# Kernel tuning notes

Hardware: AMD Instinct MI355X
Metric: run time of the kernel (lower is better)

## Reference

```python
import jax, jax.numpy as jnp
import numpy as np

LN_EPS = 1e-5


def _pos_embed_2d(w, h, c, dtype=jnp.float32):
    # matches build_2d_sincos_position_embedding: meshgrid indexing='xy' -> (h, w) grids
    grid_w = jnp.arange(w, dtype=jnp.float32)
    grid_h = jnp.arange(h, dtype=jnp.float32)
    gw, gh = jnp.meshgrid(grid_w, grid_h, indexing='xy')  # each (h, w)
    pos_dim = c // 4
    omega = 1.0 / (10000.0 ** (jnp.arange(pos_dim, dtype=jnp.float32) / pos_dim))
    out_w = gw.reshape(-1, 1) * omega[None]  # (h*w, pos_dim)
    out_h = gh.reshape(-1, 1) * omega[None]
    pe = jnp.concatenate([jnp.sin(out_w), jnp.cos(out_w), jnp.sin(out_h), jnp.cos(out_h)], axis=1)
    return pe.astype(dtype)  # (h*w, c)


def setup_inputs() -> dict:
    key = jax.random.key(0)
    k1, k2 = jax.random.split(key)
    N, C, H, W = 16, 256, 40, 40
    x = jax.random.normal(k1, (N, C, H, W), dtype=jnp.float32)
    ln_w = jnp.ones((C,), dtype=jnp.float32)
    ln_b = jnp.zeros((C,), dtype=jnp.float32)
    qkv_w = jax.random.normal(k2, (3 * C, C), dtype=jnp.float32) * 0.02  # 1x1 conv weight
    qkv_b = jnp.zeros((3 * C,), dtype=jnp.float32)
    gamma = jnp.ones((1,), dtype=jnp.float32)
    return {"x": x, "ln_w": ln_w, "ln_b": ln_b, "qkv_w": qkv_w, "qkv_b": qkv_b, "gamma": gamma}


def reference(x, ln_w, ln_b, qkv_w, qkv_b, gamma):
    N, C, H, W = x.shape
    scale = C ** (-0.5)
    identity = x

    # LayerNorm over channels (computed in NHWC like the torch permute dance)
    xh = jnp.transpose(x, (0, 2, 3, 1))  # (N, H, W, C)
    mu = jnp.mean(xh, axis=-1, keepdims=True)
    var = jnp.mean(jnp.square(xh - mu), axis=-1, keepdims=True)
    xn = (xh - mu) * jax.lax.rsqrt(var + LN_EPS) * ln_w + ln_b

    # 1x1 conv == per-pixel linear
    qkv = jnp.einsum('nhwc,oc->nhwo', xn, qkv_w) + qkv_b  # (N, H, W, 3C)
    qkv = qkv.reshape(N, H * W, 3 * C)
    q, k, v = jnp.split(qkv, 3, axis=-1)  # each (N, HW, C)

    pe = _pos_embed_2d(W, H, C, x.dtype)  # (HW, C)
    q = q + pe
    k = k + pe

    attn = jax.nn.softmax(jnp.einsum('nqc,nkc->nqk', q, k) * scale, axis=-1)
    out = jnp.einsum('nqk,nkc->nqc', attn, v)  # (N, HW, C)
    out = jnp.transpose(out, (0, 2, 1)).reshape(N, C, H, W)
    return identity + gamma[0] * out
```

## Files before the change

### kernel.cpp

```cpp
#include <hip/hip_runtime.h>
#include <hip/hip_bf16.h>

typedef float f32x4 __attribute__((ext_vector_type(4)));
typedef float f32x16 __attribute__((ext_vector_type(16)));
typedef __bf16 v8bf __attribute__((ext_vector_type(8)));
typedef unsigned short ushortx4 __attribute__((ext_vector_type(4)));
typedef unsigned short ushortx8 __attribute__((ext_vector_type(8)));
typedef unsigned int uint4v __attribute__((ext_vector_type(4)));

#define NIMG 16
#define CCH  256
#define HWP  1600
#define APIT 264

__device__ __forceinline__ unsigned short f2bf(float f) {
  unsigned int u = __builtin_bit_cast(unsigned int, f);
  u = (u + 0x7FFFu + ((u >> 16) & 1u)) >> 16;
  return (unsigned short)u;
}

__device__ __forceinline__ f32x4 mfma16(v8bf a, v8bf b, f32x4 c) {
  return __builtin_amdgcn_mfma_f32_16x16x32_bf16(a, b, c, 0, 0, 0);
}

__device__ __forceinline__ unsigned cvtpk(float a, float b) {
  unsigned r;
  asm("v_cvt_pk_bf16_f32 %0, %1, %2" : "=v"(r) : "v"(a), "v"(b));
  return r;
}
#define PSWAP(a, b) asm("v_permlane32_swap_b32 %0, %1" : "+v"(a), "+v"(b))

__global__ void prep_kernel(const float* __restrict__ qkv_w,
                            float* __restrict__ pe,
                            unsigned short* __restrict__ w_frag) {
  int tid = blockIdx.x * blockDim.x + threadIdx.x;
  int nthr = gridDim.x * blockDim.x;
  for (int i = tid; i < 768 * 256; i += nthr) {
    int o = i >> 8, c = i & 255;
    int tile = o >> 4, lr = o & 15;
    int ks = c >> 5, lg = (c >> 3) & 3, e = c & 7;
    w_frag[(((size_t)tile * 8 + ks) * 64 + lg * 16 + lr) * 8 + e] = f2bf(qkv_w[i]);
  }
  const float c1 = 9.210340371976184f / 64.f;
  for (int i = tid; i < HWP * 256; i += nthr) {
    int p = i >> 8, c = i & 255;
    int j = p % 40, ii = p / 40;
    int tt = c & 63;
    float omega = expf(-(float)tt * c1);
    float coord = (c < 128) ? (float)j : (float)ii;
    float a = coord * omega;
    pe[i] = ((c & 64) == 0) ? sinf(a) : cosf(a);
  }
}

__global__ __launch_bounds__(512, 4) void ln_qkv_kernel(
    const float* __restrict__ x, const float* __restrict__ ln_w, const float* __restrict__ ln_b,
    const unsigned short* __restrict__ w_frag, const float* __restrict__ qkv_b,
    const float* __restrict__ pe,
    unsigned short* __restrict__ q_arr, unsigned short* __restrict__ k_arr,
    unsigned short* __restrict__ v_arr) {
  __shared__ unsigned short buf[64][APIT];
  __shared__ float red_s[8][64], red_q[8][64];
  __shared__ float mu_s[64], rs_s[64];

  int t = threadIdx.x;
  int n = blockIdx.x / 25, pt = blockIdx.x % 25;
  int pix0 = pt * 64;
  int p = t & 63, g = t >> 6;
  const float* xb = x + (size_t)n * CCH * HWP + pix0;

  {
    float sum = 0.f, sq = 0.f;
#pragma unroll
    for (int i = 0; i < 32; ++i) {
      float v = xb[(size_t)(g * 32 + i) * HWP + p];
      sum += v; sq += v * v;
    }
    red_s[g][p] = sum; red_q[g][p] = sq;
  }
  __syncthreads();
  if (t < 64) {
    float s = 0.f, q2 = 0.f;
#pragma unroll
    for (int gg = 0; gg < 8; ++gg) { s += red_s[gg][t]; q2 += red_q[gg][t]; }
    float mu = s * (1.f / 256.f);
    float var = q2 * (1.f / 256.f) - mu * mu;
    mu_s[t] = mu;
    rs_s[t] = rsqrtf(var + 1e-5f);
  }
  __syncthreads();
  {
    float mu = mu_s[p], rs = rs_s[p];
#pragma unroll
    for (int i4 = 0; i4 < 8; ++i4) {
      int c0 = g * 32 + i4 * 4;
      f32x4 lw = *(const f32x4*)&ln_w[c0];
      f32x4 lb = *(const f32x4*)&ln_b[c0];
      ushortx4 pk;
#pragma unroll
      for (int r = 0; r < 4; ++r) {
        float v = xb[(size_t)(c0 + r) * HWP + p];
        pk[r] = f2bf((v - mu) * rs * lw[r] + lb[r]);
      }
      *(ushortx4*)&buf[p][c0] = pk;
    }
  }
  __syncthreads();

  int w = t >> 6, l = t & 63, lr = l & 15, lg = l >> 4;
  f32x4 acc[6][4];
#pragma unroll
  for (int nf = 0; nf < 6; ++nf)
#pragma unroll
    for (int mi = 0; mi < 4; ++mi) acc[nf][mi] = (f32x4){0.f, 0.f, 0.f, 0.f};

#pragma unroll
  for (int ks = 0; ks < 8; ++ks) {
    v8bf bF[4];
#pragma unroll
    for (int mi = 0; mi < 4; ++mi)
      bF[mi] = *(const v8bf*)&buf[mi * 16 + lr][ks * 32 + lg * 8];
#pragma unroll
    for (int nf = 0; nf < 6; ++nf) {
      int tile = w + nf * 8;
      v8bf wf = *(const v8bf*)&w_frag[(((size_t)tile * 8 + ks) * 64 + l) * 8];
#pragma unroll
      for (int mi = 0; mi < 4; ++mi) acc[nf][mi] = mfma16(wf, bF[mi], acc[nf][mi]);
    }
  }

  int lgh = lg >> 1, lgl = lg & 1;
#pragma unroll
  for (int nf = 0; nf < 2; ++nf) {
    int tile = w + nf * 8;
    f32x4 bi = *(const f32x4*)&qkv_b[tile * 16 + lg * 4];
#pragma unroll
    for (int mi = 0; mi < 4; ++mi) {
      int pix = pix0 + mi * 16 + lr;
      f32x4 pev = *(const f32x4*)&pe[(size_t)pix * 256 + tile * 16 + lg * 4];
      f32x4 vv = (acc[nf][mi] + bi + pev) * 0.0625f;
      ushortx4 pk = {f2bf(vv[0]), f2bf(vv[1]), f2bf(vv[2]), f2bf(vv[3])};
      int qt = pix >> 5, l31 = pix & 31;
      size_t ad = ((((size_t)n * 50 + qt) * 16 + tile) * 2 + lgh) * 256 + l31 * 8 + lgl * 4;
      *(ushortx4*)&q_arr[ad] = pk;
    }
  }
#pragma unroll
  for (int nf = 2; nf < 4; ++nf) {
    int tile = w + nf * 8;
    int dt = tile - 16;
    f32x4 bi = *(const f32x4*)&qkv_b[tile * 16 + lg * 4];
#pragma unroll
    for (int mi = 0; mi < 4; ++mi) {
      int pix = pix0 + mi * 16 + lr;
      f32x4 pev = *(const f32x4*)&pe[(size_t)pix * 256 + dt * 16 + lg * 4];
      f32x4 vv = acc[nf][mi] + bi + pev;
      ushortx4 pk = {f2bf(vv[0]), f2bf(vv[1]), f2bf(vv[2]), f2bf(vv[3])};
      size_t ad = (((size_t)n * 16 + dt) * 1600 + pix) * 16 + lgh * 8 + lgl * 4;
      *(ushortx4*)&k_arr[ad] = pk;
    }
  }
#pragma unroll
  for (int nf = 4; nf < 6; ++nf) {
    int tile = w + nf * 8;
    f32x4 bi = *(const f32x4*)&qkv_b[tile * 16 + lg * 4];
#pragma unroll
    for (int mi = 0; mi < 4; ++mi) {
      int pix = pix0 + mi * 16 + lr;
      int kvs = pix >> 4, hi = (pix >> 3) & 1, e = pix & 7;
      f32x4 vv = acc[nf][mi] + bi;
      size_t vb = (((size_t)n * 100 + kvs) * 2 + hi) * 2048 + e;
      int d0 = (tile - 32) * 16 + lg * 4;
#pragma unroll
      for (int r = 0; r < 4; ++r)
        v_arr[vb + (size_t)(d0 + r) * 8] = f2bf(vv[r]);
    }
  }
}

__global__ __launch_bounds__(128, 2) void attn_kernel(
    const unsigned short* __restrict__ q_arr, const unsigned short* __restrict__ k_arr,
    const unsigned short* __restrict__ v_arr, const float* __restrict__ x,
    const float* __restrict__ gamma, float* __restrict__ out) {
  __shared__ float sx[2][2][4][64][4];

  int t = threadIdx.x;
  int wv = t >> 6, l = t & 63;
  int l31 = l & 31, hi = l >> 5;
  int dto = wv * 8;
  int dto32 = wv * 4;
  int slot = blockIdx.x & 7, j = blockIdx.x >> 3;
  int n = slot + 8 * (j / 50);
  int qt = j % 50;
  int q0 = qt * 32;

  v8bf qf[8];
  {
    const unsigned short* qp = q_arr + (((size_t)n * 50 + qt) * 32 + hi) * 256 + l31 * 8;
#pragma unroll
    for (int i = 0; i < 8; ++i)
      qf[i] = *(const v8bf*)(qp + (dto + i) * 512);
  }

  f32x16 acc[4];
#pragma unroll
  for (int dd = 0; dd < 4; ++dd)
#pragma unroll
    for (int r = 0; r < 16; ++r) acc[dd][r] = 0.f;

  float m_run = -1e30f, l_run = 0.f;

  const unsigned short* kbase = k_arr + (size_t)n * (16 * 1600 * 16) +
                                (size_t)dto * 25600 + hi * 8;
  const unsigned short* vbase = v_arr + (size_t)n * (100 * 2 * 256 * 8) +
                                hi * 2048 + l31 * 8 + dto32 * 256;

  v8bf kc[8];
#pragma unroll
  for (int i = 0; i < 8; ++i)
    kc[i] = *(const v8bf*)(kbase + (size_t)i * 25600 + l31 * 16);

  for (int kt = 0; kt < 50; ++kt) {
    int pb = kt & 1;
    int ktn = (kt + 1 < 50) ? kt + 1 : 0;

    f32x16 s0, s1;
#pragma unroll
    for (int r = 0; r < 16; ++r) { s0[r] = 0.f; s1[r] = 0.f; }
#pragma unroll
    for (int i = 0; i < 8; i += 2) {
      s0 = __builtin_amdgcn_mfma_f32_32x32x16_bf16(kc[i], qf[i], s0, 0, 0, 0);
      s1 = __builtin_amdgcn_mfma_f32_32x32x16_bf16(kc[i + 1], qf[i + 1], s1, 0, 0, 0);
    }
#pragma unroll
    for (int i = 0; i < 8; ++i)
      kc[i] = *(const v8bf*)(kbase + (size_t)i * 25600 + (ktn * 32 + l31) * 16);

#pragma unroll
    for (int r4 = 0; r4 < 4; ++r4) {
      f32x4 vv = {s0[r4 * 4 + 0] + s1[r4 * 4 + 0], s0[r4 * 4 + 1] + s1[r4 * 4 + 1],
                  s0[r4 * 4 + 2] + s1[r4 * 4 + 2], s0[r4 * 4 + 3] + s1[r4 * 4 + 3]};
      *(f32x4*)&sx[pb][wv][r4][l][0] = vv;
    }

    v8bf vf0[4], vf1[4];
    {
      const unsigned short* vp = vbase + (size_t)kt * 8192;
#pragma unroll
      for (int i = 0; i < 4; ++i) vf0[i] = *(const v8bf*)(vp + i * 256);
#pragma unroll
      for (int i = 0; i < 4; ++i) vf1[i] = *(const v8bf*)(vp + 4096 + i * 256);
    }

    __syncthreads();

    float p[16];
#pragma unroll
    for (int r4 = 0; r4 < 4; ++r4) {
      f32x4 oth = *(const f32x4*)&sx[pb][wv ^ 1][r4][l][0];
#pragma unroll
      for (int rr = 0; rr < 4; ++rr)
        p[r4 * 4 + rr] = (s0[r4 * 4 + rr] + s1[r4 * 4 + rr]) + oth[rr];
    }

    float t0 = fmaxf(p[0], p[1]), t1 = fmaxf(p[2], p[3]);
    float t2 = fmaxf(p[4], p[5]), t3 = fmaxf(p[6], p[7]);
    float t4 = fmaxf(p[8], p[9]), t5 = fmaxf(p[10], p[11]);
    float t6 = fmaxf(p[12], p[13]), t7 = fmaxf(p[14], p[15]);
    float mx = fmaxf(fmaxf(fmaxf(t0, t1), fmaxf(t2, t3)),
                     fmaxf(fmaxf(t4, t5), fmaxf(t6, t7)));
    mx = fmaxf(mx, __shfl_xor(mx, 32));
    if (!__all(mx <= m_run + 2.f)) {
      float mnew = fmaxf(m_run, mx);
      float alpha = __expf(m_run - mnew);
      l_run *= alpha;
#pragma unroll
      for (int dd = 0; dd < 4; ++dd)
#pragma unroll
        for (int r = 0; r < 16; ++r) acc[dd][r] *= alpha;
      m_run = mnew;
    }
#pragma unroll
    for (int r = 0; r < 16; ++r) p[r] = __expf(p[r] - m_run);
    float sA = (p[0] + p[1]) + (p[2] + p[3]);
    float sB = (p[4] + p[5]) + (p[6] + p[7]);
    float sC = (p[8] + p[9]) + (p[10] + p[11]);
    float sD = (p[12] + p[13]) + (p[14] + p[15]);
    float sum = (sA + sB) + (sC + sD);
    sum += __shfl_xor(sum, 32);
    l_run += sum;

    unsigned x0 = cvtpk(p[0], p[1]), x1 = cvtpk(p[2], p[3]);
    unsigned y0 = cvtpk(p[4], p[5]), y1 = cvtpk(p[6], p[7]);
    PSWAP(x0, y0); PSWAP(x1, y1);
    uint4v u0 = {x0, x1, y0, y1};
    v8bf pf0 = __builtin_bit_cast(v8bf, u0);
    unsigned z0 = cvtpk(p[8], p[9]), z1 = cvtpk(p[10], p[11]);
    unsigned w0 = cvtpk(p[12], p[13]), w1 = cvtpk(p[14], p[15]);
    PSWAP(z0, w0); PSWAP(z1, w1);
    uint4v u1 = {z0, z1, w0, w1};
    v8bf pf1 = __builtin_bit_cast(v8bf, u1);

#pragma unroll
    for (int dd = 0; dd < 4; ++dd) {
      acc[dd] = __builtin_amdgcn_mfma_f32_32x32x16_bf16(vf0[dd], pf0, acc[dd], 0, 0, 0);
      acc[dd] = __builtin_amdgcn_mfma_f32_32x32x16_bf16(vf1[dd], pf1, acc[dd], 0, 0, 0);
    }
  }

  float inv = 1.f / l_run;
  float gm = gamma[0];
#pragma unroll
  for (int dd = 0; dd < 4; ++dd) {
#pragma unroll
    for (int r = 0; r < 16; ++r) {
      int d = (dto32 + dd) * 32 + (r & 3) + 8 * (r >> 2) + 4 * hi;
      size_t base = ((size_t)n * 256 + d) * HWP + q0 + l31;
      out[base] = x[base] + gm * acc[dd][r] * inv;
    }
  }
}

extern "C" void kernel_launch(void* const* d_in, const int* in_sizes, int n_in,
                              void* d_out, int out_size, void* d_ws, size_t ws_size,
                              hipStream_t stream) {
  const float* x     = (const float*)d_in[0];
  const float* ln_w  = (const float*)d_in[1];
  const float* ln_b  = (const float*)d_in[2];
  const float* qkv_w = (const float*)d_in[3];
  const float* qkv_b = (const float*)d_in[4];
  const float* gamma = (const float*)d_in[5];
  float* out = (float*)d_out;

  char* ws = (char*)d_ws;
  unsigned short* w_frag = (unsigned short*)ws;
  float*          pe     = (float*)(ws + 393216);
  unsigned short* q_arr  = (unsigned short*)(ws + 2031616);
  unsigned short* k_arr  = (unsigned short*)(ws + 15138816);
  unsigned short* v_arr  = (unsigned short*)(ws + 28246016);

  hipLaunchKernelGGL(prep_kernel, dim3(384), dim3(256), 0, stream, qkv_w, pe, w_frag);
  hipLaunchKernelGGL(ln_qkv_kernel, dim3(400), dim3(512), 0, stream,
                     x, ln_w, ln_b, w_frag, qkv_b, pe, q_arr, k_arr, v_arr);
  hipLaunchKernelGGL(attn_kernel, dim3(800), dim3(128), 0, stream,
                     q_arr, k_arr, v_arr, x, gamma, out);
}
```

Before: 128.8 us.

## Software-pipeline QK^T of next tile under softmax and fold log2e into Q

The attention loop now computes the QK^T MFMAs for tile kt+1 interleaved with the softmax and PV work of tile kt. It uses ping-pong score registers and a four-slot LDS exchange buffer, so the old per-iteration barrier sits after the next scores are already in flight. The Q prescale now includes log2(e), so the softmax can use raw v_exp_f32 (exp2) instead of __expf, with the defer threshold rescaled to match. This trades more registers and LDS for better MFMA/VALU overlap, which could reduce occupancy or cause spills.

```diff
diff --git a/kernel.cpp b/kernel.cpp
--- a/kernel.cpp
+++ b/kernel.cpp
@@ -13,6 +13,9 @@
 #define HWP  1600
 #define APIT 264
 
+#define QSCALE 0.09016844f
+#define DEFER_THR 2.885390f
+
 __device__ __forceinline__ unsigned short f2bf(float f) {
   unsigned int u = __builtin_bit_cast(unsigned int, f);
   u = (u + 0x7FFFu + ((u >> 16) & 1u)) >> 16;
@@ -26,6 +29,11 @@
 __device__ __forceinline__ unsigned cvtpk(float a, float b) {
   unsigned r;
   asm("v_cvt_pk_bf16_f32 %0, %1, %2" : "=v"(r) : "v"(a), "v"(b));
+  return r;
+}
+__device__ __forceinline__ float exp2v(float x) {
+  float r;
+  asm("v_exp_f32 %0, %1" : "=v"(r) : "v"(x));
   return r;
 }
 #define PSWAP(a, b) asm("v_permlane32_swap_b32 %0, %1" : "+v"(a), "+v"(b))
@@ -138,7 +146,7 @@
     for (int mi = 0; mi < 4; ++mi) {
       int pix = pix0 + mi * 16 + lr;
       f32x4 pev = *(const f32x4*)&pe[(size_t)pix * 256 + tile * 16 + lg * 4];
-      f32x4 vv = (acc[nf][mi] + bi + pev) * 0.0625f;
+      f32x4 vv = (acc[nf][mi] + bi + pev) * QSCALE;
       ushortx4 pk = {f2bf(vv[0]), f2bf(vv[1]), f2bf(vv[2]), f2bf(vv[3])};
       int qt = pix >> 5, l31 = pix & 31;
       size_t ad = ((((size_t)n * 50 + qt) * 16 + tile) * 2 + lgh) * 256 + l31 * 8 + lgl * 4;
@@ -182,7 +190,7 @@
     const unsigned short* __restrict__ q_arr, const unsigned short* __restrict__ k_arr,
     const unsigned short* __restrict__ v_arr, const float* __restrict__ x,
     const float* __restrict__ gamma, float* __restrict__ out) {
-  __shared__ float sx[2][2][4][64][4];
+  __shared__ float sx[4][2][4][64][4];
 
   int t = threadIdx.x;
   int wv = t >> 6, l = t & 63;
@@ -220,49 +228,46 @@
   for (int i = 0; i < 8; ++i)
     kc[i] = *(const v8bf*)(kbase + (size_t)i * 25600 + l31 * 16);
 
-  for (int kt = 0; kt < 50; ++kt) {
-    int pb = kt & 1;
-    int ktn = (kt + 1 < 50) ? kt + 1 : 0;
-
-    f32x16 s0, s1;
-#pragma unroll
-    for (int r = 0; r < 16; ++r) { s0[r] = 0.f; s1[r] = 0.f; }
-#pragma unroll
-    for (int i = 0; i < 8; i += 2) {
-      s0 = __builtin_amdgcn_mfma_f32_32x32x16_bf16(kc[i], qf[i], s0, 0, 0, 0);
-      s1 = __builtin_amdgcn_mfma_f32_32x32x16_bf16(kc[i + 1], qf[i + 1], s1, 0, 0, 0);
-    }
-#pragma unroll
-    for (int i = 0; i < 8; ++i)
-      kc[i] = *(const v8bf*)(kbase + (size_t)i * 25600 + (ktn * 32 + l31) * 16);
-
+  f32x16 sA, sB;
+#pragma unroll
+  for (int r = 0; r < 16; ++r) sA[r] = 0.f;
+#pragma unroll
+  for (int i = 0; i < 8; ++i)
+    sA = __builtin_amdgcn_mfma_f32_32x32x16_bf16(kc[i], qf[i], sA, 0, 0, 0);
+
+#pragma unroll
+  for (int r4 = 0; r4 < 4; ++r4) {
+    f32x4 vv = {sA[r4 * 4 + 0], sA[r4 * 4 + 1], sA[r4 * 4 + 2], sA[r4 * 4 + 3]};
+    *(f32x4*)&sx[0][wv][r4][l][0] = vv;
+  }
+#pragma unroll
+  for (int i = 0; i < 8; ++i)
+    kc[i] = *(const v8bf*)(kbase + (size_t)i * 25600 + (32 + l31) * 16);
+
+  v8bf vf0[4], vf1[4];
+#pragma unroll
+  for (int i = 0; i < 4; ++i) vf0[i] = *(const v8bf*)(vbase + i * 256);
+#pragma unroll
+  for (int i = 0; i < 4; ++i) vf1[i] = *(const v8bf*)(vbase + 4096 + i * 256);
+
+  auto body = [&](int kt, f32x16& scur, f32x16& snxt, bool nexttile) {
+    __syncthreads();
+    int br = kt & 3;
+    float p[16];
 #pragma unroll
     for (int r4 = 0; r4 < 4; ++r4) {
-      f32x4 vv = {s0[r4 * 4 + 0] + s1[r4 * 4 + 0], s0[r4 * 4 + 1] + s1[r4 * 4 + 1],
-                  s0[r4 * 4 + 2] + s1[r4 * 4 + 2], s0[r4 * 4 + 3] + s1[r4 * 4 + 3]};
-      *(f32x4*)&sx[pb][wv][r4][l][0] = vv;
-    }
-
-    v8bf vf0[4], vf1[4];
-    {
-      const unsigned short* vp = vbase + (size_t)kt * 8192;
-#pragma unroll
-      for (int i = 0; i < 4; ++i) vf0[i] = *(const v8bf*)(vp + i * 256);
-#pragma unroll
-      for (int i = 0; i < 4; ++i) vf1[i] = *(const v8bf*)(vp + 4096 + i * 256);
-    }
-
-    __syncthreads();
-
-    float p[16];
-#pragma unroll
-    for (int r4 = 0; r4 < 4; ++r4) {
-      f32x4 oth = *(const f32x4*)&sx[pb][wv ^ 1][r4][l][0];
+      f32x4 oth = *(const f32x4*)&sx[br][wv ^ 1][r4][l][0];
 #pragma unroll
       for (int rr = 0; rr < 4; ++rr)
-        p[r4 * 4 + rr] = (s0[r4 * 4 + rr] + s1[r4 * 4 + rr]) + oth[rr];
-    }
-
+        p[r4 * 4 + rr] = scur[r4 * 4 + rr] + oth[rr];
+    }
+    if (nexttile) {
+#pragma unroll
+      for (int r = 0; r < 16; ++r) snxt[r] = 0.f;
+#pragma unroll
+      for (int i = 0; i < 4; ++i)
+        snxt = __builtin_amdgcn_mfma_f32_32x32x16_bf16(kc[i], qf[i], snxt, 0, 0, 0);
+    }
     float t0 = fmaxf(p[0], p[1]), t1 = fmaxf(p[2], p[3]);
     float t2 = fmaxf(p[4], p[5]), t3 = fmaxf(p[6], p[7]);
     float t4 = fmaxf(p[8], p[9]), t5 = fmaxf(p[10], p[11]);
@@ -270,9 +275,9 @@
     float mx = fmaxf(fmaxf(fmaxf(t0, t1), fmaxf(t2, t3)),
                      fmaxf(fmaxf(t4, t5), fmaxf(t6, t7)));
     mx = fmaxf(mx, __shfl_xor(mx, 32));
-    if (!__all(mx <= m_run + 2.f)) {
+    if (!__all(mx <= m_run + DEFER_THR)) {
       float mnew = fmaxf(m_run, mx);
-      float alpha = __expf(m_run - mnew);
+      float alpha = exp2v(m_run - mnew);
       l_run *= alpha;
 #pragma unroll
       for (int dd = 0; dd < 4; ++dd)
@@ -280,15 +285,17 @@
         for (int r = 0; r < 16; ++r) acc[dd][r] *= alpha;
       m_run = mnew;
     }
-#pragma unroll
-    for (int r = 0; r < 16; ++r) p[r] = __expf(p[r] - m_run);
-    float sA = (p[0] + p[1]) + (p[2] + p[3]);
-    float sB = (p[4] + p[5]) + (p[6] + p[7]);
-    float sC = (p[8] + p[9]) + (p[10] + p[11]);
-    float sD = (p[12] + p[13]) + (p[14] + p[15]);
-    float sum = (sA + sB) + (sC + sD);
-    sum += __shfl_xor(sum, 32);
-    l_run += sum;
+    if (nexttile) {
+#pragma unroll
+      for (int i = 4; i < 8; ++i)
+        snxt = __builtin_amdgcn_mfma_f32_32x32x16_bf16(kc[i], qf[i], snxt, 0, 0, 0);
+    }
+#pragma unroll
+    for (int r = 0; r < 16; ++r) p[r] = exp2v(p[r] - m_run);
+    float sSum = ((p[0] + p[1]) + (p[2] + p[3])) + ((p[4] + p[5]) + (p[6] + p[7])) +
+                 (((p[8] + p[9]) + (p[10] + p[11])) + ((p[12] + p[13]) + (p[14] + p[15])));
+    sSum += __shfl_xor(sSum, 32);
+    l_run += sSum;
 
     unsigned x0 = cvtpk(p[0], p[1]), x1 = cvtpk(p[2], p[3]);
     unsigned y0 = cvtpk(p[4], p[5]), y1 = cvtpk(p[6], p[7]);
@@ -306,7 +313,32 @@
       acc[dd] = __builtin_amdgcn_mfma_f32_32x32x16_bf16(vf0[dd], pf0, acc[dd], 0, 0, 0);
       acc[dd] = __builtin_amdgcn_mfma_f32_32x32x16_bf16(vf1[dd], pf1, acc[dd], 0, 0, 0);
     }
-  }
+
+    if (nexttile) {
+      int bw = (kt + 1) & 3;
+#pragma unroll
+      for (int r4 = 0; r4 < 4; ++r4) {
+        f32x4 vv = {snxt[r4 * 4 + 0], snxt[r4 * 4 + 1], snxt[r4 * 4 + 2], snxt[r4 * 4 + 3]};
+        *(f32x4*)&sx[bw][wv][r4][l][0] = vv;
+      }
+      int kt2 = (kt + 2 < 50) ? kt + 2 : 0;
+#pragma unroll
+      for (int i = 0; i < 8; ++i)
+        kc[i] = *(const v8bf*)(kbase + (size_t)i * 25600 + (kt2 * 32 + l31) * 16);
+      const unsigned short* vp = vbase + (size_t)(kt + 1) * 8192;
+#pragma unroll
+      for (int i = 0; i < 4; ++i) vf0[i] = *(const v8bf*)(vp + i * 256);
+#pragma unroll
+      for (int i = 0; i < 4; ++i) vf1[i] = *(const v8bf*)(vp + 4096 + i * 256);
+    }
+  };
+
+  for (int kt = 0; kt < 48; kt += 2) {
+    body(kt, sA, sB, true);
+    body(kt + 1, sB, sA, true);
+  }
+  body(48, sA, sB, true);
+  body(49, sB, sA, false);
 
   float inv = 1.f / l_run;
   float gm = gamma[0];
```

Result: faster. 122.7 us (-4.8%).
